# Performance work log

Measured on AMD Instinct MI355X. Metric: run time of the kernel, lower is better.

The kernel has to match this reference:

```python
import jax, jax.numpy as jnp
import numpy as np
from jax import lax

D_MODEL = 256
SCALES = 3
DM2 = 2 * D_MODEL            # 512, inner d_model of each Mamba2
EXPAND = 2
D_INNER = EXPAND * DM2       # 1024
HEADDIM = 64                 # Mamba2 default
NHEADS = D_INNER // HEADDIM  # 16
DSTATE = 128
DCONV = 4
D_IN_PROJ = 2 * D_INNER + 2 * DSTATE + NHEADS  # 2320
CONV_CH = D_INNER + 2 * DSTATE                 # 1280


def layernorm(x, g, b, eps=1e-5):
    mu = x.mean(-1, keepdims=True)
    v = ((x - mu) ** 2).mean(-1, keepdims=True)
    return (x - mu) * lax.rsqrt(v + eps) * g + b


def mamba2(x, Win, convw, convb, dtb, Alog, Dh, normw, Wout):
    # x: [B, L, DM2]
    Bb, L, _ = x.shape
    zxbcdt = x @ Win                                   # [B, L, 2320]
    z = zxbcdt[..., :D_INNER]                          # gate branch
    xBC = zxbcdt[..., D_INNER:D_INNER + CONV_CH]       # [B, L, 1280]
    dt = jax.nn.softplus(zxbcdt[..., -NHEADS:] + dtb)  # [B, L, H]
    # causal depthwise conv1d over time
    xc = lax.conv_general_dilated(
        xBC.transpose(0, 2, 1), convw[:, None, :], (1,), [(DCONV - 1, 0)],
        feature_group_count=CONV_CH, dimension_numbers=('NCH', 'OIH', 'NCH'))
    xBC = jax.nn.silu(xc.transpose(0, 2, 1) + convb)
    xs = xBC[..., :D_INNER].reshape(Bb, L, NHEADS, HEADDIM)  # [B,L,H,P]
    Bm = xBC[..., D_INNER:D_INNER + DSTATE]                  # [B,L,N] (ngroups=1)
    Cm = xBC[..., D_INNER + DSTATE:]                         # [B,L,N]
    A = -jnp.exp(Alog)                                       # [H]
    dA = jnp.exp(dt * A)                                     # [B,L,H]

    def step(h, inp):
        dA_t, dt_t, x_t, B_t, C_t = inp
        h = dA_t[:, :, None, None] * h + jnp.einsum('bh,bhp,bn->bhpn', dt_t, x_t, B_t)
        return h, jnp.einsum('bhpn,bn->bhp', h, C_t)

    h0 = jnp.zeros((Bb, NHEADS, HEADDIM, DSTATE), x.dtype)
    _, ys = lax.scan(step, h0, (dA.transpose(1, 0, 2), dt.transpose(1, 0, 2),
                                xs.transpose(1, 0, 2, 3), Bm.transpose(1, 0, 2),
                                Cm.transpose(1, 0, 2)))
    y = ys.transpose(1, 0, 2, 3) + Dh[None, None, :, None] * xs   # skip term
    y = y.reshape(Bb, L, D_INNER)
    y = y * jax.nn.silu(z)                                        # gated RMSNorm
    y = y * lax.rsqrt((y * y).mean(-1, keepdims=True) + 1e-5) * normw
    return y @ Wout


def msfusion(x, Wp, bp, Wpre, bpre, lnpre_g, lnpre_b, Wpost, bpost, lnpost_g, lnpost_b,
             Win_f, convw_f, convb_f, dtb_f, Alog_f, Dh_f, normw_f, Wout_f,
             Win_b, convw_b, convb_b, dtb_b, Alog_b, Dh_b, normw_b, Wout_b):
    B, S, T, D = x.shape
    x_ = x.transpose(0, 2, 1, 3).reshape(B, T, S * D)
    x_ = x_ @ Wp + bp                                  # 1x1 conv == linear
    shortcut = x_
    h = layernorm(x_ @ Wpre + bpre, lnpre_g, lnpre_b)  # [B,T,512]
    gate = jax.nn.silu(h)
    out_f = mamba2(h, Win_f, convw_f, convb_f, dtb_f, Alog_f, Dh_f, normw_f, Wout_f)
    out_b = jnp.flip(mamba2(jnp.flip(h, 1), Win_b, convw_b, convb_b, dtb_b, Alog_b, Dh_b, normw_b, Wout_b), 1)
    out = layernorm((out_f * gate + out_b * gate) @ Wpost + bpost, lnpost_g, lnpost_b) + shortcut
    fn = out / jnp.maximum(jnp.linalg.norm(out, axis=-1, keepdims=True), 1e-12)
    attn = jnp.einsum('btd,bsd->bts', fn, fn)          # [B,T,T]
    return out, attn


def setup_inputs() -> dict:
    key = jax.random.key(0)
    ks = iter(jax.random.split(key, 40))
    n = lambda shape, s=0.02: (s * jax.random.normal(next(ks), shape)).astype(jnp.float32)
    B, S, T, D = 4, SCALES, 2048, D_MODEL
    inp = {
        'x': jax.random.normal(next(ks), (B, S, T, D), jnp.float32),
        'Wp': n((S * D, D)), 'bp': n((D,)),
        'Wpre': n((D, DM2)), 'bpre': n((DM2,)),
        'lnpre_g': jnp.ones((DM2,), jnp.float32), 'lnpre_b': jnp.zeros((DM2,), jnp.float32),
        'Wpost': n((DM2, D)), 'bpost': n((D,)),
        'lnpost_g': jnp.ones((D,), jnp.float32), 'lnpost_b': jnp.zeros((D,), jnp.float32),
    }
    for sfx in ('f', 'b'):
        inp['Win_' + sfx] = n((DM2, D_IN_PROJ))
        inp['convw_' + sfx] = n((CONV_CH, DCONV), 0.1)
        inp['convb_' + sfx] = jnp.zeros((CONV_CH,), jnp.float32)
        inp['dtb_' + sfx] = n((NHEADS,), 0.5)
        inp['Alog_' + sfx] = jnp.log(jnp.arange(1, NHEADS + 1, dtype=jnp.float32))
        inp['Dh_' + sfx] = jnp.ones((NHEADS,), jnp.float32)
        inp['normw_' + sfx] = jnp.ones((D_INNER,), jnp.float32)
        inp['Wout_' + sfx] = n((D_INNER, DM2))
    return inp


def reference(x, Wp, bp, Wpre, bpre, lnpre_g, lnpre_b, Wpost, bpost, lnpost_g, lnpost_b,
              Win_f, convw_f, convb_f, dtb_f, Alog_f, Dh_f, normw_f, Wout_f,
              Win_b, convw_b, convb_b, dtb_b, Alog_b, Dh_b, normw_b, Wout_b):
    return msfusion(x, Wp, bp, Wpre, bpre, lnpre_g, lnpre_b, Wpost, bpost, lnpost_g, lnpost_b,
                    Win_f, convw_f, convb_f, dtb_f, Alog_f, Dh_f, normw_f, Wout_f,
                    Win_b, convw_b, convb_b, dtb_b, Alog_b, Dh_b, normw_b, Wout_b)
```

## Files before the change

kernel.cpp:

```cpp
#include <hip/hip_runtime.h>
#include <math.h>

__device__ __forceinline__ float sigf(float v) { return 1.f / (1.f + __expf(-v)); }

__device__ __forceinline__ short f2bf(float f) {
  unsigned int u = __builtin_bit_cast(unsigned int, f);
  unsigned int r = (u + 0x7fffu + ((u >> 16) & 1u)) >> 16;
  return (short)r;
}
__device__ __forceinline__ float bf2f(short s) {
  unsigned int u = ((unsigned int)(unsigned short)s) << 16;
  return __builtin_bit_cast(float, u);
}

typedef short bf16x8 __attribute__((ext_vector_type(8)));
typedef float f32x4 __attribute__((ext_vector_type(4)));

__device__ __forceinline__ void async16(const short* g, short* l) {
  __builtin_amdgcn_global_load_lds(
      (const __attribute__((address_space(1))) unsigned int*)g,
      (__attribute__((address_space(3))) unsigned int*)l, 16, 0, 0);
}

template<bool BIAS, bool ACC>
__global__ __launch_bounds__(256) void gemm16_kernel(
    const short* __restrict__ A, const short* __restrict__ Bt,
    const float* __restrict__ bias, float* __restrict__ C,
    int M, int N, int K, int ldc,
    long long sAb, long long sBb, long long sCb)
{
  __shared__ short sm[2][2][128 * 32];
  const int tid = threadIdx.x;
  const int wave = tid >> 6;
  const int lane = tid & 63;
  const int m0 = blockIdx.x * 128;
  const int n0 = blockIdx.y * 128;
  const int bz = blockIdx.z;
  const short* Ab = A + (size_t)bz * sAb;
  const short* Bb = Bt + (size_t)bz * sBb;
  float* Cb = C + (size_t)bz * sCb;

  f32x4 acc[4][4] = {};

  const int isB = wave >> 1;
  const int half = wave & 1;
  const short* gsrc = isB ? Bb : Ab;
  const int tile_r0 = isB ? n0 : m0;
  const int lrow = lane >> 2;
  const int lk = (((lane & 3) ^ ((lane >> 3) & 3)) * 8);
  const short* gbase = gsrc + (size_t)(tile_r0 + half * 64 + lrow) * K + lk;
  short* lbase0 = &sm[0][isB][(half * 64) * 32];
  short* lbase1 = &sm[1][isB][(half * 64) * 32];

  const int wm = wave >> 1, wn = wave & 1;
  const int nt = K >> 5;

  auto STAGE = [&](int buf, int t) {
    const short* g0 = gbase + t * 32;
    short* l0 = buf ? lbase1 : lbase0;
#pragma unroll
    for (int c = 0; c < 4; c++)
      async16(g0 + (size_t)c * 16 * K, l0 + c * 512);
  };

  STAGE(0, 0);
  asm volatile("s_waitcnt vmcnt(0)" ::: "memory");
  __builtin_amdgcn_s_barrier();

  const int rs = (((lane >> 4) ^ ((lane >> 1) & 3)) * 8);
  int cur = 0;
  for (int t = 0; t < nt; ++t) {
    if (t + 1 < nt) STAGE(cur ^ 1, t + 1);
    const short* smA = &sm[cur][0][0];
    const short* smB = &sm[cur][1][0];
    bf16x8 af[4], bfr[4];
#pragma unroll
    for (int mt = 0; mt < 4; mt++)
      af[mt] = *(bf16x8*)&smA[(wm * 64 + mt * 16 + (lane & 15)) * 32 + rs];
#pragma unroll
    for (int nn = 0; nn < 4; nn++)
      bfr[nn] = *(bf16x8*)&smB[(wn * 64 + nn * 16 + (lane & 15)) * 32 + rs];
#pragma unroll
    for (int mt = 0; mt < 4; mt++)
#pragma unroll
      for (int nn = 0; nn < 4; nn++)
        acc[mt][nn] = __builtin_amdgcn_mfma_f32_16x16x32_bf16(bfr[nn], af[mt], acc[mt][nn], 0, 0, 0);
    asm volatile("s_waitcnt vmcnt(0)" ::: "memory");
    __builtin_amdgcn_s_barrier();
    cur ^= 1;
  }
  const int mcol = lane & 15;
  const int nq = (lane >> 4) * 4;
#pragma unroll
  for (int mt = 0; mt < 4; mt++) {
    int row = m0 + wm * 64 + mt * 16 + mcol;
#pragma unroll
    for (int nn = 0; nn < 4; nn++) {
      int col = n0 + wn * 64 + nn * 16 + nq;
      if (col >= N) continue;
      float4 v = make_float4(acc[mt][nn][0], acc[mt][nn][1], acc[mt][nn][2], acc[mt][nn][3]);
      float* cp = Cb + (size_t)row * ldc + col;
      if (BIAS) {
        float4 bv = *(const float4*)(bias + col);
        v.x += bv.x; v.y += bv.y; v.z += bv.z; v.w += bv.w;
      }
      if (ACC) {
        float4 ov = *(const float4*)cp;
        v.x += ov.x; v.y += ov.y; v.z += ov.z; v.w += ov.w;
      }
      *(float4*)cp = v;
    }
  }
}

__global__ void tcast_kernel(const float* __restrict__ W, short* __restrict__ Wt,
                             int K, int N)
{
  __shared__ float tile[32][33];
  int n0 = blockIdx.x * 32, k0 = blockIdx.y * 32;
  int c = threadIdx.x & 31, r8 = threadIdx.x >> 5;
#pragma unroll
  for (int i = 0; i < 4; i++) {
    int r = r8 + i * 8;
    int n = n0 + c;
    tile[r][c] = (n < N) ? W[(size_t)(k0 + r) * N + n] : 0.f;
  }
  __syncthreads();
#pragma unroll
  for (int i = 0; i < 4; i++) {
    int r = r8 + i * 8;
    Wt[(size_t)(n0 + r) * K + k0 + c] = f2bf(tile[c][r]);
  }
}

__global__ void gather_cast_kernel(const float* __restrict__ x, short* __restrict__ Ag)
{
  int idx = blockIdx.x * 256 + threadIdx.x;
  int m = idx / 192;
  int g = idx - m * 192;
  int k = g * 4;
  int s = k >> 8, d = k & 255;
  int b = m >> 11, t = m & 2047;
  float4 v = *(const float4*)(x + ((size_t)((b * 3 + s) * 2048 + t) << 8) + d);
  *(short4*)(Ag + (size_t)m * 768 + k) = make_short4(f2bf(v.x), f2bf(v.y), f2bf(v.z), f2bf(v.w));
}

__global__ void cast_kernel(const float* __restrict__ in, short* __restrict__ out)
{
  size_t idx = (size_t)blockIdx.x * 256 + threadIdx.x;
  float4 v = *(const float4*)(in + idx * 4);
  *(short4*)(out + idx * 4) = make_short4(f2bf(v.x), f2bf(v.y), f2bf(v.z), f2bf(v.w));
}

__global__ void ln512_kernel(float* __restrict__ xio, const float* __restrict__ g,
                             const float* __restrict__ b, short* __restrict__ o16)
{
  const int row = blockIdx.x;
  const int lane = threadIdx.x;
  float* xr = xio + (size_t)row * 512;
  float4 v0 = *(float4*)(xr + lane * 4);
  float4 v1 = *(float4*)(xr + 256 + lane * 4);
  float sum = v0.x + v0.y + v0.z + v0.w + v1.x + v1.y + v1.z + v1.w;
#pragma unroll
  for (int o = 32; o >= 1; o >>= 1) sum += __shfl_xor(sum, o);
  const float mu = sum * (1.f / 512.f);
  float d[8] = {v0.x - mu, v0.y - mu, v0.z - mu, v0.w - mu,
                v1.x - mu, v1.y - mu, v1.z - mu, v1.w - mu};
  float vs = 0.f;
#pragma unroll
  for (int i = 0; i < 8; i++) vs += d[i] * d[i];
#pragma unroll
  for (int o = 32; o >= 1; o >>= 1) vs += __shfl_xor(vs, o);
  const float inv = rsqrtf(vs * (1.f / 512.f) + 1e-5f);
  float4 g0 = *(const float4*)(g + lane * 4);
  float4 g1 = *(const float4*)(g + 256 + lane * 4);
  float4 b0 = *(const float4*)(b + lane * 4);
  float4 b1 = *(const float4*)(b + 256 + lane * 4);
  v0.x = d[0] * inv * g0.x + b0.x; v0.y = d[1] * inv * g0.y + b0.y;
  v0.z = d[2] * inv * g0.z + b0.z; v0.w = d[3] * inv * g0.w + b0.w;
  v1.x = d[4] * inv * g1.x + b1.x; v1.y = d[5] * inv * g1.y + b1.y;
  v1.z = d[6] * inv * g1.z + b1.z; v1.w = d[7] * inv * g1.w + b1.w;
  *(float4*)(xr + lane * 4) = v0;
  *(float4*)(xr + 256 + lane * 4) = v1;
  short* orow = o16 + (size_t)row * 512;
  *(short4*)(orow + lane * 4) = make_short4(f2bf(v0.x), f2bf(v0.y), f2bf(v0.z), f2bf(v0.w));
  *(short4*)(orow + 256 + lane * 4) = make_short4(f2bf(v1.x), f2bf(v1.y), f2bf(v1.z), f2bf(v1.w));
}

__global__ void dtprep_kernel(const float* __restrict__ Z, const float* __restrict__ dtb,
                              const float* __restrict__ Alog,
                              float* __restrict__ dtv, float* __restrict__ ldA)
{
  int idx = blockIdx.x * 256 + threadIdx.x;
  int row = idx >> 4, hh = idx & 15;
  float raw = Z[(size_t)row * 2320 + 2304 + hh] + dtb[hh];
  float dt = raw > 20.f ? raw : log1pf(expf(raw));
  dtv[idx] = dt;
  ldA[idx] = -dt * expf(Alog[hh]);
}

__global__ void conv_kernel(const float* __restrict__ Z, const float* __restrict__ convw,
                            const float* __restrict__ convb, short* __restrict__ xcv, int dir)
{
  int row = blockIdx.x;
  int c = blockIdx.y * 256 + threadIdx.x;
  int t = row & 2047;
  size_t bbase = (size_t)(row - t) * 2320;
  float wv[4] = {convw[c * 4 + 0], convw[c * 4 + 1], convw[c * 4 + 2], convw[c * 4 + 3]};
  float acc = convb[c];
#pragma unroll
  for (int k = 0; k < 4; k++) {
    int ts = dir ? (t + 3 - k) : (t - 3 + k);
    if (ts >= 0 && ts < 2048)
      acc += wv[k] * Z[bbase + (size_t)ts * 2320 + 1024 + c];
  }
  xcv[(size_t)row * 1280 + c] = f2bf(acc * sigf(acc));
}

__global__ __launch_bounds__(256) void chunk_state_kernel(
    const short* __restrict__ xcv, const float* __restrict__ dtv,
    const float* __restrict__ ldA, short* __restrict__ Sbuf,
    float* __restrict__ Pbuf, int dir)
{
  __shared__ float sw[64];
  __shared__ short sXT[64 * 72];
  __shared__ short sBw[128 * 72];
  const int bh = blockIdx.x, ck = blockIdx.y;
  const int b = bh >> 4, h = bh & 15;
  const int tid = threadIdx.x;
  const int wave = tid >> 6, lane = tid & 63;

  if (tid < 64) {
    int tg = ck * 64 + tid;
    int tt = dir ? 2047 - tg : tg;
    size_t r = (size_t)(b * 2048 + tt) * 16 + h;
    float v = ldA[r];
#pragma unroll
    for (int o = 1; o < 64; o <<= 1) { float u = __shfl_up(v, o); if (tid >= o) v += u; }
    float tot = __shfl(v, 63);
    sw[tid] = __expf(tot - v) * dtv[r];
    if (tid == 63) Pbuf[bh * 32 + ck] = __expf(tot);
  }
  __syncthreads();
  for (int i4 = tid; i4 < 512; i4 += 256) {
    int s = i4 >> 3, p0 = (i4 & 7) * 8;
    int tg = ck * 64 + s; int tt = dir ? 2047 - tg : tg;
    bf16x8 xv = *(const bf16x8*)(xcv + (size_t)(b * 2048 + tt) * 1280 + h * 64 + p0);
#pragma unroll
    for (int j = 0; j < 8; j++) sXT[(p0 + j) * 72 + s] = xv[j];
  }
  for (int i4 = tid; i4 < 1024; i4 += 256) {
    int s = i4 >> 4, n0 = (i4 & 15) * 8;
    int tg = ck * 64 + s; int tt = dir ? 2047 - tg : tg;
    bf16x8 bv = *(const bf16x8*)(xcv + (size_t)(b * 2048 + tt) * 1280 + 1024 + n0);
    float w = sw[s];
#pragma unroll
    for (int j = 0; j < 8; j++) sBw[(n0 + j) * 72 + s] = f2bf(w * bf2f(bv[j]));
  }
  __syncthreads();

  const int mcol = lane & 15, kgrp = (lane >> 4) * 8;
  bf16x8 af[2];
#pragma unroll
  for (int kk = 0; kk < 2; kk++)
    af[kk] = *(bf16x8*)&sXT[(wave * 16 + mcol) * 72 + kk * 32 + kgrp];
  f32x4 acc[8] = {};
#pragma unroll
  for (int j = 0; j < 8; j++)
#pragma unroll
    for (int kk = 0; kk < 2; kk++) {
      bf16x8 bf = *(bf16x8*)&sBw[(j * 16 + mcol) * 72 + kk * 32 + kgrp];
      acc[j] = __builtin_amdgcn_mfma_f32_16x16x32_bf16(bf, af[kk], acc[j], 0, 0, 0);
    }
  short* Sp = Sbuf + ((size_t)(bh * 32 + ck) << 13);
  const int p = wave * 16 + mcol;
  const int nq = (lane >> 4) * 4;
#pragma unroll
  for (int j = 0; j < 8; j++) {
    *(short4*)(Sp + p * 128 + j * 16 + nq) = make_short4(
        f2bf(acc[j][0]), f2bf(acc[j][1]), f2bf(acc[j][2]), f2bf(acc[j][3]));
  }
}

__global__ void chunk_scan_kernel(short* __restrict__ Sbuf, const float* __restrict__ Pbuf)
{
  int idx = blockIdx.x * 256 + threadIdx.x;
  int bh = idx >> 12, pr = idx & 4095;
  float h0 = 0.f, h1 = 0.f;
  for (int ck = 0; ck < 32; ck++) {
    size_t off = ((size_t)(bh * 32 + ck) << 13) + pr * 2;
    unsigned int u = *(const unsigned int*)(Sbuf + off);
    float s0 = bf2f((short)(u & 0xffff));
    float s1 = bf2f((short)(u >> 16));
    float P = Pbuf[bh * 32 + ck];
    unsigned int w = (unsigned int)(unsigned short)f2bf(h0) |
                     ((unsigned int)(unsigned short)f2bf(h1) << 16);
    *(unsigned int*)(Sbuf + off) = w;
    h0 = P * h0 + s0;
    h1 = P * h1 + s1;
  }
}

__global__ __launch_bounds__(256) void chunk_out_kernel(
    const short* __restrict__ xcv, const float* __restrict__ dtv,
    const float* __restrict__ ldA, const short* __restrict__ Sbuf,
    const float* __restrict__ Dh, short* __restrict__ y, int dir)
{
  extern __shared__ short smem16[];
  short* sC  = smem16;
  short* sB  = sC + 64 * 136;
  short* sH  = sB + 64 * 136;
  short* sXT = sH + 64 * 136;
  short* sP  = sXT + 64 * 72;
  float* sL  = (float*)(sP + 64 * 72);
  float* sdt = sL + 64;

  const int bh = blockIdx.x, ck = blockIdx.y;
  const int b = bh >> 4, h = bh & 15;
  const int tid = threadIdx.x;
  const int wave = tid >> 6, lane = tid & 63;

  if (tid < 64) {
    int tg = ck * 64 + tid;
    int tt = dir ? 2047 - tg : tg;
    size_t r = (size_t)(b * 2048 + tt) * 16 + h;
    float v = ldA[r];
#pragma unroll
    for (int o = 1; o < 64; o <<= 1) { float u = __shfl_up(v, o); if (tid >= o) v += u; }
    sL[tid] = v;
    sdt[tid] = dtv[r];
  }
  for (int i4 = tid; i4 < 1024; i4 += 256) {
    int t = i4 >> 4, c8 = (i4 & 15) * 8;
    int tg = ck * 64 + t; int tt = dir ? 2047 - tg : tg;
    const short* rp = xcv + (size_t)(b * 2048 + tt) * 1280;
    *(bf16x8*)&sB[t * 136 + c8] = *(const bf16x8*)(rp + 1024 + c8);
    *(bf16x8*)&sC[t * 136 + c8] = *(const bf16x8*)(rp + 1152 + c8);
  }
  for (int i4 = tid; i4 < 512; i4 += 256) {
    int t = i4 >> 3, p0 = (i4 & 7) * 8;
    int tg = ck * 64 + t; int tt = dir ? 2047 - tg : tg;
    bf16x8 xv = *(const bf16x8*)(xcv + (size_t)(b * 2048 + tt) * 1280 + h * 64 + p0);
#pragma unroll
    for (int j = 0; j < 8; j++) sXT[(p0 + j) * 72 + t] = xv[j];
  }
  const short* Hp = Sbuf + ((size_t)(bh * 32 + ck) << 13);
  for (int i4 = tid; i4 < 1024; i4 += 256) {
    int p = i4 >> 4, c8 = (i4 & 15) * 8;
    *(bf16x8*)&sH[p * 136 + c8] = *(const bf16x8*)(Hp + p * 128 + c8);
  }
  __syncthreads();

  const int mcol = lane & 15;
  const int kgrp = (lane >> 4) * 8;
  const int trow = wave * 16 + mcol;
  const int sq = (lane >> 4) * 4;

  bf16x8 afC[4];
#pragma unroll
  for (int kk = 0; kk < 4; kk++)
    afC[kk] = *(bf16x8*)&sC[trow * 136 + kk * 32 + kgrp];

  f32x4 sacc[4] = {};
#pragma unroll
  for (int j = 0; j < 4; j++)
#pragma unroll
    for (int kk = 0; kk < 4; kk++) {
      bf16x8 bf = *(bf16x8*)&sB[(j * 16 + mcol) * 136 + kk * 32 + kgrp];
      sacc[j] = __builtin_amdgcn_mfma_f32_16x16x32_bf16(bf, afC[kk], sacc[j], 0, 0, 0);
    }

  const float Lt = sL[trow];
#pragma unroll
  for (int j = 0; j < 4; j++) {
    int s0 = j * 16 + sq;
    float vr[4];
#pragma unroll
    for (int r = 0; r < 4; r++) {
      int s = s0 + r;
      vr[r] = (trow >= s) ? sacc[j][r] * __expf(Lt - sL[s]) * sdt[s] : 0.f;
    }
    *(short4*)&sP[trow * 72 + s0] = make_short4(
        f2bf(vr[0]), f2bf(vr[1]), f2bf(vr[2]), f2bf(vr[3]));
  }
  __syncthreads();

  bf16x8 afP[2];
#pragma unroll
  for (int kk = 0; kk < 2; kk++)
    afP[kk] = *(bf16x8*)&sP[trow * 72 + kk * 32 + kgrp];
  f32x4 yacc[4] = {};
#pragma unroll
  for (int j = 0; j < 4; j++)
#pragma unroll
    for (int kk = 0; kk < 2; kk++) {
      bf16x8 bf = *(bf16x8*)&sXT[(j * 16 + mcol) * 72 + kk * 32 + kgrp];
      yacc[j] = __builtin_amdgcn_mfma_f32_16x16x32_bf16(bf, afP[kk], yacc[j], 0, 0, 0);
    }
  f32x4 y2[4] = {};
#pragma unroll
  for (int j = 0; j < 4; j++)
#pragma unroll
    for (int kk = 0; kk < 4; kk++) {
      bf16x8 bf = *(bf16x8*)&sH[(j * 16 + mcol) * 136 + kk * 32 + kgrp];
      y2[j] = __builtin_amdgcn_mfma_f32_16x16x32_bf16(bf, afC[kk], y2[j], 0, 0, 0);
    }

  const float dh = Dh[h];
  const float eL = __expf(Lt);
  const int tg = ck * 64 + trow;
  const int tt = dir ? 2047 - tg : tg;
  short* yrow = y + (size_t)(b * 2048 + tt) * 1024 + h * 64;
#pragma unroll
  for (int j = 0; j < 4; j++) {
    int p0 = j * 16 + sq;
    short o[4];
#pragma unroll
    for (int r = 0; r < 4; r++) {
      float xv = bf2f(sXT[(p0 + r) * 72 + trow]);
      o[r] = f2bf(yacc[j][r] + eL * y2[j][r] + dh * xv);
    }
    *(short4*)(yrow + p0) = make_short4(o[0], o[1], o[2], o[3]);
  }
}

__global__ void rms_kernel(short* __restrict__ y, const float* __restrict__ Z,
                           const float* __restrict__ normw)
{
  const int row = blockIdx.x;
  const int lane = threadIdx.x;
  short* yr = y + (size_t)row * 1024;
  const float* zr = Z + (size_t)row * 2320;
  float vals[16];
  float ss = 0.f;
#pragma unroll
  for (int jj = 0; jj < 4; jj++) {
    int off = jj * 256 + lane * 4;
    short4 yv = *(short4*)(yr + off);
    float4 zv = *(const float4*)(zr + off);
    float a0 = bf2f(yv.x) * (zv.x * sigf(zv.x));
    float a1 = bf2f(yv.y) * (zv.y * sigf(zv.y));
    float a2 = bf2f(yv.z) * (zv.z * sigf(zv.z));
    float a3 = bf2f(yv.w) * (zv.w * sigf(zv.w));
    vals[jj * 4 + 0] = a0; vals[jj * 4 + 1] = a1;
    vals[jj * 4 + 2] = a2; vals[jj * 4 + 3] = a3;
    ss += a0 * a0 + a1 * a1 + a2 * a2 + a3 * a3;
  }
#pragma unroll
  for (int o = 32; o >= 1; o >>= 1) ss += __shfl_xor(ss, o);
  const float scale = rsqrtf(ss * (1.f / 1024.f) + 1e-5f);
#pragma unroll
  for (int jj = 0; jj < 4; jj++) {
    int off = jj * 256 + lane * 4;
    float4 nw = *(const float4*)(normw + off);
    *(short4*)(yr + off) = make_short4(
        f2bf(vals[jj * 4 + 0] * scale * nw.x), f2bf(vals[jj * 4 + 1] * scale * nw.y),
        f2bf(vals[jj * 4 + 2] * scale * nw.z), f2bf(vals[jj * 4 + 3] * scale * nw.w));
  }
}

__global__ void combine_kernel(const float* __restrict__ od, const float* __restrict__ h,
                               short* __restrict__ ob)
{
  size_t idx = (size_t)blockIdx.x * 256 + threadIdx.x;
  float4 o = ((const float4*)od)[idx];
  float4 g = ((const float4*)h)[idx];
  o.x *= g.x * sigf(g.x);
  o.y *= g.y * sigf(g.y);
  o.z *= g.z * sigf(g.z);
  o.w *= g.w * sigf(g.w);
  *(short4*)(ob + idx * 4) = make_short4(f2bf(o.x), f2bf(o.y), f2bf(o.z), f2bf(o.w));
}

__global__ void lnshort_kernel(const float* __restrict__ v, const float* __restrict__ g,
                               const float* __restrict__ b, const float* __restrict__ shortcut,
                               float* __restrict__ out0, short* __restrict__ fn)
{
  const int row = blockIdx.x;
  const int lane = threadIdx.x;
  size_t base = (size_t)row * 256;
  float4 x = *(const float4*)(v + base + lane * 4);
  float sum = x.x + x.y + x.z + x.w;
#pragma unroll
  for (int o = 32; o >= 1; o >>= 1) sum += __shfl_xor(sum, o);
  const float mu = sum * (1.f / 256.f);
  float d[4] = {x.x - mu, x.y - mu, x.z - mu, x.w - mu};
  float vs = d[0] * d[0] + d[1] * d[1] + d[2] * d[2] + d[3] * d[3];
#pragma unroll
  for (int o = 32; o >= 1; o >>= 1) vs += __shfl_xor(vs, o);
  const float inv = rsqrtf(vs * (1.f / 256.f) + 1e-5f);
  float4 gg = *(const float4*)(g + lane * 4);
  float4 bb = *(const float4*)(b + lane * 4);
  float4 sc = *(const float4*)(shortcut + base + lane * 4);
  float4 o4;
  o4.x = d[0] * inv * gg.x + bb.x + sc.x;
  o4.y = d[1] * inv * gg.y + bb.y + sc.y;
  o4.z = d[2] * inv * gg.z + bb.z + sc.z;
  o4.w = d[3] * inv * gg.w + bb.w + sc.w;
  *(float4*)(out0 + base + lane * 4) = o4;
  float ns = o4.x * o4.x + o4.y * o4.y + o4.z * o4.z + o4.w * o4.w;
#pragma unroll
  for (int o = 32; o >= 1; o >>= 1) ns += __shfl_xor(ns, o);
  const float r = 1.f / fmaxf(sqrtf(ns), 1e-12f);
  *(short4*)(fn + base + lane * 4) =
      make_short4(f2bf(o4.x * r), f2bf(o4.y * r), f2bf(o4.z * r), f2bf(o4.w * r));
}

extern "C" void kernel_launch(void* const* d_in, const int* in_sizes, int n_in,
                              void* d_out, int out_size, void* d_ws, size_t ws_size,
                              hipStream_t stream)
{
  (void)in_sizes; (void)n_in; (void)out_size; (void)ws_size;
  const float* x        = (const float*)d_in[0];
  const float* Wp       = (const float*)d_in[1];
  const float* bp       = (const float*)d_in[2];
  const float* Wpre     = (const float*)d_in[3];
  const float* bpre     = (const float*)d_in[4];
  const float* lnpre_g  = (const float*)d_in[5];
  const float* lnpre_b  = (const float*)d_in[6];
  const float* Wpost    = (const float*)d_in[7];
  const float* bpost    = (const float*)d_in[8];
  const float* lnpost_g = (const float*)d_in[9];
  const float* lnpost_b = (const float*)d_in[10];

  float* ws   = (float*)d_ws;
  float* Zb   = ws;
  float* xcvr = Zb + 19005440;
  float* xc   = xcvr + 10485760;
  float* hbuf = xc + 2097152;
  short* hb16 = (short*)(hbuf + 4194304);
  float* yb16f= hbuf + 4194304 + 2097152;
  short* yb16 = (short*)yb16f;
  float* od   = yb16f + 4194304;
  float* dtv  = od + 4194304;
  float* ldA  = dtv + 131072;
  float* Pbuf = ldA + 131072;
  short* WinT = (short*)(Pbuf + 2048);
  short* WoutT= WinT + 1245184;

  short* xcv16  = (short*)xcvr;
  short* Ag16   = (short*)xcvr;
  short* WpT    = (short*)(xcvr + 3145728);
  short* xcb    = (short*)xcvr;
  short* WpreT  = (short*)(xcvr + 1048576);
  short* ob16   = (short*)xcvr;
  short* WpostT = (short*)(xcvr + 2097152);
  float* vbuf = yb16f;
  short* fn16 = (short*)(yb16f + 2097152);

  float* out0 = (float*)d_out;
  float* attn = out0 + 2097152;
  short* Sbuf16 = (short*)attn;

  tcast_kernel<<<dim3(8, 24), 256, 0, stream>>>(Wp, WpT, 768, 256);
  gather_cast_kernel<<<6144, 256, 0, stream>>>(x, Ag16);
  gemm16_kernel<true, false><<<dim3(64, 2), 256, 0, stream>>>(Ag16, WpT, bp, xc, 8192, 256, 768, 256, 0, 0, 0);
  cast_kernel<<<2048, 256, 0, stream>>>(xc, xcb);
  tcast_kernel<<<dim3(16, 8), 256, 0, stream>>>(Wpre, WpreT, 256, 512);
  gemm16_kernel<true, false><<<dim3(64, 4), 256, 0, stream>>>(xcb, WpreT, bpre, hbuf, 8192, 512, 256, 512, 0, 0, 0);
  ln512_kernel<<<8192, 64, 0, stream>>>(hbuf, lnpre_g, lnpre_b, hb16);

  for (int dir = 0; dir < 2; dir++) {
    const float* Win   = (const float*)d_in[11 + dir * 8];
    const float* convw = (const float*)d_in[12 + dir * 8];
    const float* convb = (const float*)d_in[13 + dir * 8];
    const float* dtb   = (const float*)d_in[14 + dir * 8];
    const float* Alog  = (const float*)d_in[15 + dir * 8];
    const float* Dh    = (const float*)d_in[16 + dir * 8];
    const float* normw = (const float*)d_in[17 + dir * 8];
    const float* Wout  = (const float*)d_in[18 + dir * 8];

    tcast_kernel<<<dim3(76, 16), 256, 0, stream>>>(Win, WinT, 512, 2320);
    tcast_kernel<<<dim3(16, 32), 256, 0, stream>>>(Wout, WoutT, 1024, 512);
    gemm16_kernel<false, false><<<dim3(64, 19), 256, 0, stream>>>(hb16, WinT, nullptr, Zb, 8192, 2320, 512, 2320, 0, 0, 0);
    dtprep_kernel<<<512, 256, 0, stream>>>(Zb, dtb, Alog, dtv, ldA);
    conv_kernel<<<dim3(8192, 5), 256, 0, stream>>>(Zb, convw, convb, xcv16, dir);
    chunk_state_kernel<<<dim3(64, 32), 256, 0, stream>>>(xcv16, dtv, ldA, Sbuf16, Pbuf, dir);
    chunk_scan_kernel<<<1024, 256, 0, stream>>>(Sbuf16, Pbuf);
    chunk_out_kernel<<<dim3(64, 32), 256, 71168, stream>>>(xcv16, dtv, ldA, Sbuf16, Dh, yb16, dir);
    rms_kernel<<<8192, 64, 0, stream>>>(yb16, Zb, normw);
    if (dir == 0)
      gemm16_kernel<false, false><<<dim3(64, 4), 256, 0, stream>>>(yb16, WoutT, nullptr, od, 8192, 512, 1024, 512, 0, 0, 0);
    else
      gemm16_kernel<false, true><<<dim3(64, 4), 256, 0, stream>>>(yb16, WoutT, nullptr, od, 8192, 512, 1024, 512, 0, 0, 0);
  }

  combine_kernel<<<4096, 256, 0, stream>>>(od, hbuf, ob16);
  tcast_kernel<<<dim3(8, 16), 256, 0, stream>>>(Wpost, WpostT, 512, 256);
  gemm16_kernel<true, false><<<dim3(64, 2), 256, 0, stream>>>(ob16, WpostT, bpost, vbuf, 8192, 256, 512, 256, 0, 0, 0);
  lnshort_kernel<<<8192, 64, 0, stream>>>(vbuf, lnpost_g, lnpost_b, xc, out0, fn16);
  gemm16_kernel<false, false><<<dim3(16, 16, 4), 256, 0, stream>>>(
      fn16, fn16, nullptr, attn, 2048, 2048, 256, 2048,
      (long long)2048 * 256, (long long)2048 * 256, (long long)2048 * 2048);
}
```

Baseline: 630.0 us.

## Batch forward and backward Mamba2 directions into single kernel launches

Replaces the per-direction loop with kernels that process both directions at once through an extra grid dimension. Workspace buffers (Z, xcv, Sbuf, y, dt, ldA, Pbuf, transposed weights) are duplicated per direction and addressed by fixed strides. This doubles the parallelism per launch and halves the launch count, which targets underfilled grids such as the chunk kernels. The cost is a larger workspace footprint and more memory pressure. The Sbuf region aliased into the output buffer now spans twice the size, which is a risk if that region is too small.

```diff
diff --git a/kernel.cpp b/kernel.cpp
--- a/kernel.cpp
+++ b/kernel.cpp
@@ -15,6 +15,13 @@
 
 typedef short bf16x8 __attribute__((ext_vector_type(8)));
 typedef float f32x4 __attribute__((ext_vector_type(4)));
+
+#define ZB_STRIDE   19005440ll
+#define XCV_STRIDE  10485760ll
+#define SBUF_STRIDE 16777216ll
+#define YB_STRIDE    8388608ll
+#define DT_STRIDE     131072ll
+#define PB_STRIDE       2048ll
 
 __device__ __forceinline__ void async16(const short* g, short* l) {
   __builtin_amdgcn_global_load_lds(
@@ -133,6 +140,29 @@
   }
 }
 
+__global__ void tcast2_kernel(const float* __restrict__ W0, const float* __restrict__ W1,
+                              short* __restrict__ Wt, int K, int N, long long sWt)
+{
+  __shared__ float tile[32][33];
+  const int dir = blockIdx.z;
+  const float* W = dir ? W1 : W0;
+  short* Wtd = Wt + (size_t)dir * sWt;
+  int n0 = blockIdx.x * 32, k0 = blockIdx.y * 32;
+  int c = threadIdx.x & 31, r8 = threadIdx.x >> 5;
+#pragma unroll
+  for (int i = 0; i < 4; i++) {
+    int r = r8 + i * 8;
+    int n = n0 + c;
+    tile[r][c] = (n < N) ? W[(size_t)(k0 + r) * N + n] : 0.f;
+  }
+  __syncthreads();
+#pragma unroll
+  for (int i = 0; i < 4; i++) {
+    int r = r8 + i * 8;
+    Wtd[(size_t)(n0 + r) * K + k0 + c] = f2bf(tile[c][r]);
+  }
+}
+
 __global__ void gather_cast_kernel(const float* __restrict__ x, short* __restrict__ Ag)
 {
   int idx = blockIdx.x * 256 + threadIdx.x;
@@ -187,21 +217,35 @@
   *(short4*)(orow + 256 + lane * 4) = make_short4(f2bf(v1.x), f2bf(v1.y), f2bf(v1.z), f2bf(v1.w));
 }
 
-__global__ void dtprep_kernel(const float* __restrict__ Z, const float* __restrict__ dtb,
-                              const float* __restrict__ Alog,
+__global__ void dtprep_kernel(const float* __restrict__ Z,
+                              const float* __restrict__ dtb0, const float* __restrict__ dtb1,
+                              const float* __restrict__ Alog0, const float* __restrict__ Alog1,
                               float* __restrict__ dtv, float* __restrict__ ldA)
 {
+  const int dir = blockIdx.y;
+  const float* Zd = Z + (size_t)dir * ZB_STRIDE;
+  const float* dtb = dir ? dtb1 : dtb0;
+  const float* Alog = dir ? Alog1 : Alog0;
+  float* dtvd = dtv + dir * DT_STRIDE;
+  float* ldAd = ldA + dir * DT_STRIDE;
   int idx = blockIdx.x * 256 + threadIdx.x;
   int row = idx >> 4, hh = idx & 15;
-  float raw = Z[(size_t)row * 2320 + 2304 + hh] + dtb[hh];
+  float raw = Zd[(size_t)row * 2320 + 2304 + hh] + dtb[hh];
   float dt = raw > 20.f ? raw : log1pf(expf(raw));
-  dtv[idx] = dt;
-  ldA[idx] = -dt * expf(Alog[hh]);
-}
-
-__global__ void conv_kernel(const float* __restrict__ Z, const float* __restrict__ convw,
-                            const float* __restrict__ convb, short* __restrict__ xcv, int dir)
-{
+  dtvd[idx] = dt;
+  ldAd[idx] = -dt * expf(Alog[hh]);
+}
+
+__global__ void conv_kernel(const float* __restrict__ Z,
+                            const float* __restrict__ cw0, const float* __restrict__ cw1,
+                            const float* __restrict__ cb0, const float* __restrict__ cb1,
+                            short* __restrict__ xcv)
+{
+  const int dir = blockIdx.z;
+  const float* Zd = Z + (size_t)dir * ZB_STRIDE;
+  short* xd = xcv + (size_t)dir * XCV_STRIDE;
+  const float* convw = dir ? cw1 : cw0;
+  const float* convb = dir ? cb1 : cb0;
   int row = blockIdx.x;
   int c = blockIdx.y * 256 + threadIdx.x;
   int t = row & 2047;
@@ -212,19 +256,25 @@
   for (int k = 0; k < 4; k++) {
     int ts = dir ? (t + 3 - k) : (t - 3 + k);
     if (ts >= 0 && ts < 2048)
-      acc += wv[k] * Z[bbase + (size_t)ts * 2320 + 1024 + c];
-  }
-  xcv[(size_t)row * 1280 + c] = f2bf(acc * sigf(acc));
+      acc += wv[k] * Zd[bbase + (size_t)ts * 2320 + 1024 + c];
+  }
+  xd[(size_t)row * 1280 + c] = f2bf(acc * sigf(acc));
 }
 
 __global__ __launch_bounds__(256) void chunk_state_kernel(
-    const short* __restrict__ xcv, const float* __restrict__ dtv,
-    const float* __restrict__ ldA, short* __restrict__ Sbuf,
-    float* __restrict__ Pbuf, int dir)
+    const short* __restrict__ xcv_, const float* __restrict__ dtv_,
+    const float* __restrict__ ldA_, short* __restrict__ Sbuf_,
+    float* __restrict__ Pbuf_)
 {
   __shared__ float sw[64];
   __shared__ short sXT[64 * 72];
   __shared__ short sBw[128 * 72];
+  const int dir = blockIdx.z;
+  const short* xcv = xcv_ + (size_t)dir * XCV_STRIDE;
+  const float* dtv = dtv_ + dir * DT_STRIDE;
+  const float* ldA = ldA_ + dir * DT_STRIDE;
+  short* Sbuf = Sbuf_ + (size_t)dir * SBUF_STRIDE;
+  float* Pbuf = Pbuf_ + dir * PB_STRIDE;
   const int bh = blockIdx.x, ck = blockIdx.y;
   const int b = bh >> 4, h = bh & 15;
   const int tid = threadIdx.x;
@@ -285,26 +335,31 @@
 __global__ void chunk_scan_kernel(short* __restrict__ Sbuf, const float* __restrict__ Pbuf)
 {
   int idx = blockIdx.x * 256 + threadIdx.x;
-  int bh = idx >> 12, pr = idx & 4095;
+  int bhd = idx >> 12;
+  int pr = idx & 4095;
+  int dir = bhd >> 6, bh = bhd & 63;
+  short* Sb = Sbuf + (size_t)dir * SBUF_STRIDE;
+  const float* Pb = Pbuf + dir * PB_STRIDE;
   float h0 = 0.f, h1 = 0.f;
   for (int ck = 0; ck < 32; ck++) {
     size_t off = ((size_t)(bh * 32 + ck) << 13) + pr * 2;
-    unsigned int u = *(const unsigned int*)(Sbuf + off);
+    unsigned int u = *(const unsigned int*)(Sb + off);
     float s0 = bf2f((short)(u & 0xffff));
     float s1 = bf2f((short)(u >> 16));
-    float P = Pbuf[bh * 32 + ck];
+    float P = Pb[bh * 32 + ck];
     unsigned int w = (unsigned int)(unsigned short)f2bf(h0) |
                      ((unsigned int)(unsigned short)f2bf(h1) << 16);
-    *(unsigned int*)(Sbuf + off) = w;
+    *(unsigned int*)(Sb + off) = w;
     h0 = P * h0 + s0;
     h1 = P * h1 + s1;
   }
 }
 
 __global__ __launch_bounds__(256) void chunk_out_kernel(
-    const short* __restrict__ xcv, const float* __restrict__ dtv,
-    const float* __restrict__ ldA, const short* __restrict__ Sbuf,
-    const float* __restrict__ Dh, short* __restrict__ y, int dir)
+    const short* __restrict__ xcv_, const float* __restrict__ dtv_,
+    const float* __restrict__ ldA_, const short* __restrict__ Sbuf_,
+    const float* __restrict__ Dh0, const float* __restrict__ Dh1,
+    short* __restrict__ y_)
 {
   extern __shared__ short smem16[];
   short* sC  = smem16;
@@ -315,6 +370,14 @@
   float* sL  = (float*)(sP + 64 * 72);
   float* sdt = sL + 64;
 
+  const int dir = blockIdx.z;
+  const short* xcv = xcv_ + (size_t)dir * XCV_STRIDE;
+  const float* dtv = dtv_ + dir * DT_STRIDE;
+  const float* ldA = ldA_ + dir * DT_STRIDE;
+  const short* Sbuf = Sbuf_ + (size_t)dir * SBUF_STRIDE;
+  const float* Dh = dir ? Dh1 : Dh0;
+  short* y = y_ + (size_t)dir * YB_STRIDE;
+
   const int bh = blockIdx.x, ck = blockIdx.y;
   const int b = bh >> 4, h = bh & 15;
   const int tid = threadIdx.x;
@@ -424,13 +487,15 @@
   }
 }
 
-__global__ void rms_kernel(short* __restrict__ y, const float* __restrict__ Z,
-                           const float* __restrict__ normw)
-{
+__global__ void rms_kernel(short* __restrict__ y_, const float* __restrict__ Z,
+                           const float* __restrict__ nw0, const float* __restrict__ nw1)
+{
+  const int dir = blockIdx.y;
   const int row = blockIdx.x;
   const int lane = threadIdx.x;
-  short* yr = y + (size_t)row * 1024;
-  const float* zr = Z + (size_t)row * 2320;
+  short* yr = y_ + (size_t)dir * YB_STRIDE + (size_t)row * 1024;
+  const float* zr = Z + (size_t)dir * ZB_STRIDE + (size_t)row * 2320;
+  const float* normw = dir ? nw1 : nw0;
   float vals[16];
   float ss = 0.f;
 #pragma unroll
@@ -522,21 +587,37 @@
   const float* bpost    = (const float*)d_in[8];
   const float* lnpost_g = (const float*)d_in[9];
   const float* lnpost_b = (const float*)d_in[10];
+  const float* Win_f   = (const float*)d_in[11];
+  const float* convw_f = (const float*)d_in[12];
+  const float* convb_f = (const float*)d_in[13];
+  const float* dtb_f   = (const float*)d_in[14];
+  const float* Alog_f  = (const float*)d_in[15];
+  const float* Dh_f    = (const float*)d_in[16];
+  const float* normw_f = (const float*)d_in[17];
+  const float* Wout_f  = (const float*)d_in[18];
+  const float* Win_b   = (const float*)d_in[19];
+  const float* convw_b = (const float*)d_in[20];
+  const float* convb_b = (const float*)d_in[21];
+  const float* dtb_b   = (const float*)d_in[22];
+  const float* Alog_b  = (const float*)d_in[23];
+  const float* Dh_b    = (const float*)d_in[24];
+  const float* normw_b = (const float*)d_in[25];
+  const float* Wout_b  = (const float*)d_in[26];
 
   float* ws   = (float*)d_ws;
   float* Zb   = ws;
-  float* xcvr = Zb + 19005440;
+  float* xcvr = Zb + 2 * 19005440;
   float* xc   = xcvr + 10485760;
   float* hbuf = xc + 2097152;
   short* hb16 = (short*)(hbuf + 4194304);
   float* yb16f= hbuf + 4194304 + 2097152;
   short* yb16 = (short*)yb16f;
-  float* od   = yb16f + 4194304;
+  float* od   = yb16f + 8388608;
   float* dtv  = od + 4194304;
-  float* ldA  = dtv + 131072;
-  float* Pbuf = ldA + 131072;
-  short* WinT = (short*)(Pbuf + 2048);
-  short* WoutT= WinT + 1245184;
+  float* ldA  = dtv + 262144;
+  float* Pbuf = ldA + 262144;
+  short* WinT = (short*)(Pbuf + 4096);
+  short* WoutT= WinT + 2 * 1245184;
 
   short* xcv16  = (short*)xcvr;
   short* Ag16   = (short*)xcvr;
@@ -560,30 +641,18 @@
   gemm16_kernel<true, false><<<dim3(64, 4), 256, 0, stream>>>(xcb, WpreT, bpre, hbuf, 8192, 512, 256, 512, 0, 0, 0);
   ln512_kernel<<<8192, 64, 0, stream>>>(hbuf, lnpre_g, lnpre_b, hb16);
 
-  for (int dir = 0; dir < 2; dir++) {
-    const float* Win   = (const float*)d_in[11 + dir * 8];
-    const float* convw = (const float*)d_in[12 + dir * 8];
-    const float* convb = (const float*)d_in[13 + dir * 8];
-    const float* dtb   = (const float*)d_in[14 + dir * 8];
-    const float* Alog  = (const float*)d_in[15 + dir * 8];
-    const float* Dh    = (const float*)d_in[16 + dir * 8];
-    const float* normw = (const float*)d_in[17 + dir * 8];
-    const float* Wout  = (const float*)d_in[18 + dir * 8];
-
-    tcast_kernel<<<dim3(76, 16), 256, 0, stream>>>(Win, WinT, 512, 2320);
-    tcast_kernel<<<dim3(16, 32), 256, 0, stream>>>(Wout, WoutT, 1024, 512);
-    gemm16_kernel<false, false><<<dim3(64, 19), 256, 0, stream>>>(hb16, WinT, nullptr, Zb, 8192, 2320, 512, 2320, 0, 0, 0);
-    dtprep_kernel<<<512, 256, 0, stream>>>(Zb, dtb, Alog, dtv, ldA);
-    conv_kernel<<<dim3(8192, 5), 256, 0, stream>>>(Zb, convw, convb, xcv16, dir);
-    chunk_state_kernel<<<dim3(64, 32), 256, 0, stream>>>(xcv16, dtv, ldA, Sbuf16, Pbuf, dir);
-    chunk_scan_kernel<<<1024, 256, 0, stream>>>(Sbuf16, Pbuf);
-    chunk_out_kernel<<<dim3(64, 32), 256, 71168, stream>>>(xcv16, dtv, ldA, Sbuf16, Dh, yb16, dir);
-    rms_kernel<<<8192, 64, 0, stream>>>(yb16, Zb, normw);
-    if (dir == 0)
-      gemm16_kernel<false, false><<<dim3(64, 4), 256, 0, stream>>>(yb16, WoutT, nullptr, od, 8192, 512, 1024, 512, 0, 0, 0);
-    else
-      gemm16_kernel<false, true><<<dim3(64, 4), 256, 0, stream>>>(yb16, WoutT, nullptr, od, 8192, 512, 1024, 512, 0, 0, 0);
-  }
+  tcast2_kernel<<<dim3(76, 16, 2), 256, 0, stream>>>(Win_f, Win_b, WinT, 512, 2320, 1245184);
+  tcast2_kernel<<<dim3(16, 32, 2), 256, 0, stream>>>(Wout_f, Wout_b, WoutT, 1024, 512, 524288);
+  gemm16_kernel<false, false><<<dim3(64, 19, 2), 256, 0, stream>>>(
+      hb16, WinT, nullptr, Zb, 8192, 2320, 512, 2320, 0, 1245184, ZB_STRIDE);
+  dtprep_kernel<<<dim3(512, 2), 256, 0, stream>>>(Zb, dtb_f, dtb_b, Alog_f, Alog_b, dtv, ldA);
+  conv_kernel<<<dim3(8192, 5, 2), 256, 0, stream>>>(Zb, convw_f, convw_b, convb_f, convb_b, xcv16);
+  chunk_state_kernel<<<dim3(64, 32, 2), 256, 0, stream>>>(xcv16, dtv, ldA, Sbuf16, Pbuf);
+  chunk_scan_kernel<<<2048, 256, 0, stream>>>(Sbuf16, Pbuf);
+  chunk_out_kernel<<<dim3(64, 32, 2), 256, 71168, stream>>>(xcv16, dtv, ldA, Sbuf16, Dh_f, Dh_b, yb16);
+  rms_kernel<<<dim3(8192, 2), 64, 0, stream>>>(yb16, Zb, normw_f, normw_b);
+  gemm16_kernel<false, false><<<dim3(64, 4), 256, 0, stream>>>(yb16, WoutT, nullptr, od, 8192, 512, 1024, 512, 0, 0, 0);
+  gemm16_kernel<false, true><<<dim3(64, 4), 256, 0, stream>>>(yb16 + YB_STRIDE, WoutT + 524288, nullptr, od, 8192, 512, 1024, 512, 0, 0, 0);
 
   combine_kernel<<<4096, 256, 0, stream>>>(od, hbuf, ob16);
   tcast_kernel<<<dim3(8, 16), 256, 0, stream>>>(Wpost, WpostT, 512, 256);
```

New measurement: 612.1 us. 2.8% less time.
